# Performance work log

Hardware: AMD Instinct MI355X
Metric: run time of the kernel (lower is better)

Reference implementation:

```python
import jax, jax.numpy as jnp
import numpy as np

B = 16          # frames in batch
N = 16384       # atoms (num_nodes)
R = 1024        # residues (segments)
D = 320         # input_dim
BINS = 32       # adaptive-pool feature bins (output_size_per_segment[1])
H = 512         # mlp_hidden_dim
COND = 3        # conditioner dim (X_ref)
EPS = 1e-5


def setup_inputs() -> dict:
    key = jax.random.key(0)
    ks = jax.random.split(key, 8)
    x = jax.random.normal(ks[0], (B * N, D), dtype=jnp.float32)
    cond = jax.random.normal(ks[1], (N, COND), dtype=jnp.float32)
    # sorted residue ids -> contiguous variable-size segments, like real residues
    seg_ids = jnp.sort(jax.random.randint(ks[2], (N,), 0, R, dtype=jnp.int32))
    W1 = jax.random.normal(ks[3], (BINS + COND, H), dtype=jnp.float32) * 0.05
    b1 = jnp.zeros((H,), jnp.float32)
    gamma = jnp.ones((H,), jnp.float32)
    beta = jnp.zeros((H,), jnp.float32)
    bn_mean = jnp.zeros((H,), jnp.float32)
    bn_var = jnp.ones((H,), jnp.float32)
    W2 = jax.random.normal(ks[4], (H, 3), dtype=jnp.float32) * 0.05
    b2 = jnp.zeros((3,), jnp.float32)
    return {"x": x, "cond": cond, "seg_ids": seg_ids, "W1": W1, "b1": b1,
            "gamma": gamma, "beta": beta, "bn_mean": bn_mean, "bn_var": bn_var,
            "W2": W2, "b2": b2}


def reference(x, cond, seg_ids, W1, b1, gamma, beta, bn_mean, bn_var, W2, b2):
    # x: [B*N, D] atom embeddings
    x3 = x.reshape(B, N, D)
    # --- per-residue AdaptiveAvgPool2d((1, BINS)) as a fused segment mean ---
    # output height 1 == mean over all atoms of the residue
    counts = jax.ops.segment_sum(jnp.ones((N,), x.dtype), seg_ids, num_segments=R)
    sums = jax.vmap(lambda xb: jax.ops.segment_sum(xb, seg_ids, num_segments=R))(x3)  # [B,R,D]
    seg_mean = sums / jnp.maximum(counts, 1.0)[None, :, None]
    # adaptive width D -> BINS (D divisible by BINS => exact chunk means)
    pooled = seg_mean.reshape(B, R, BINS, D // BINS).mean(-1)  # [B,R,BINS]
    # --- broadcast residue feature back to atoms, concat conditioner ---
    per_atom = pooled[:, seg_ids, :]                           # [B,N,BINS]
    cond_b = jnp.broadcast_to(cond[None], (B, N, COND))
    feat = jnp.concatenate([per_atom, cond_b], axis=-1).reshape(B * N, BINS + COND)
    # --- decoder MLP: Linear -> ReLU -> BatchNorm1d(eval) -> Linear ---
    h = jnp.maximum(feat @ W1 + b1, 0.0)
    h = (h - bn_mean) * jax.lax.rsqrt(bn_var + EPS) * gamma + beta
    out = h @ W2 + b2                                          # [B*N, 3]
    return out
```

## Files before the change

### kernel.cpp

```cpp
#include <hip/hip_runtime.h>
#include <math.h>

#define B_ 16
#define N_ 16384
#define R_ 1024
#define D_ 320
#define BINS_ 32
#define H_ 512
#define EPS_ 1e-5f
#define AP 516
#define EP 260

__global__ __launch_bounds__(256) void k_prep(const int* __restrict__ seg,
                      const float* __restrict__ gamma, const float* __restrict__ beta,
                      const float* __restrict__ mean, const float* __restrict__ var,
                      const float* __restrict__ W2, const float* __restrict__ b2,
                      int* __restrict__ off, float* __restrict__ W2f,
                      float* __restrict__ bias3, float* __restrict__ pooled){
  __shared__ float red[3 * 256];
  int blk = blockIdx.x, tid = threadIdx.x;
  if (blk < 5){
    int g = blk * 256 + tid;
    if (g <= R_){
      int lo = 0, hi = N_;
      while (lo < hi){ int mid = (lo + hi) >> 1; if (seg[mid] < g) lo = mid + 1; else hi = mid; }
      off[g] = lo;
    }
  } else if (blk == 5){
    float p0 = 0.f, p1 = 0.f, p2 = 0.f;
    for (int h = tid; h < H_; h += 256){
      float c = gamma[h] / sqrtf(var[h] + EPS_);
      float d = beta[h] - mean[h] * c;
      float w0 = W2[h * 3 + 0], w1 = W2[h * 3 + 1], w2 = W2[h * 3 + 2];
      W2f[h * 3 + 0] = c * w0; W2f[h * 3 + 1] = c * w1; W2f[h * 3 + 2] = c * w2;
      p0 += d * w0; p1 += d * w1; p2 += d * w2;
    }
    red[tid] = p0; red[256 + tid] = p1; red[512 + tid] = p2;
    __syncthreads();
    for (int s = 128; s > 0; s >>= 1){
      if (tid < s){
        red[tid] += red[tid + s];
        red[256 + tid] += red[256 + tid + s];
        red[512 + tid] += red[512 + tid + s];
      }
      __syncthreads();
    }
    if (tid < 3) bias3[tid] = b2[tid] + red[tid * 256];
  } else {
    float4 z = {0.f, 0.f, 0.f, 0.f};
    float4* p4 = (float4*)pooled;
    const int total4 = B_ * R_ * BINS_ / 4;
    for (int i = (blk - 6) * 256 + tid; i < total4; i += 32 * 256) p4[i] = z;
  }
}

__global__ __launch_bounds__(256) void k_pool(const float* __restrict__ x,
                                              const int* __restrict__ seg,
                                              float* __restrict__ pooled){
  __shared__ __align__(16) float red[4 * 320];
  int tid = threadIdx.x;
  int wid = tid >> 6, lane = tid & 63;
  int c = blockIdx.x * 4 + wid;
  int b = blockIdx.y;
  int base = c * 64;
  int my_seg = seg[base + lane];
  int prev = __shfl_up(my_seg, 1);
  bool bnd = (lane == 0) || (my_seg != prev);
  unsigned long long mask = __ballot(bnd);
  const float* xp = x + ((size_t)b * N_ + base) * D_ + lane;
  float* wred = &red[wid * 320];
  while (mask){
    int i = __builtin_ctzll(mask);
    mask &= mask - 1;
    int e = mask ? __builtin_ctzll(mask) : 64;
    int sg = __shfl(my_seg, i);
    float a0 = 0.f, a1 = 0.f, a2 = 0.f, a3 = 0.f, a4 = 0.f;
    const float* rp = xp + (size_t)i * D_;
    for (int r = i; r < e; r++, rp += D_){
      a0 += rp[0]; a1 += rp[64]; a2 += rp[128]; a3 += rp[192]; a4 += rp[256];
    }
    wred[lane] = a0; wred[64 + lane] = a1; wred[128 + lane] = a2;
    wred[192 + lane] = a3; wred[256 + lane] = a4;
    if (lane < 32){
      float s = 0.f;
      #pragma unroll
      for (int j = 0; j < 10; j++) s += wred[lane * 10 + j];
      atomicAdd(&pooled[((size_t)b * R_ + sg) * BINS_ + lane], s);
    }
  }
}

__global__ __launch_bounds__(256) void k_main(const float* __restrict__ pooled, const float* __restrict__ cond,
                      const float* __restrict__ W1, const float* __restrict__ b1,
                      const int* __restrict__ off, const float* __restrict__ W2f,
                      const float* __restrict__ bias3, float* __restrict__ out){
  __shared__ __align__(16) float P[B_ * BINS_];
  __shared__ __align__(16) float A[B_ * AP];
  __shared__ __align__(16) float E[16 * EP];
  __shared__ float condT[16 * 3];
  int tid = threadIdx.x;
  int r = blockIdx.x;
  int s = off[r];
  int cnt = off[r + 1] - s;
  if (cnt == 0) return;

  float sc = 1.0f / (float)(cnt * 10);
  for (int i = tid; i < B_ * BINS_; i += 256)
    P[i] = pooled[(size_t)((i >> 5) * R_ + r) * BINS_ + (i & 31)] * sc;
  __syncthreads();

  for (int h = tid; h < H_; h += 256){
    float bb = b1[h];
    float acc[B_];
    #pragma unroll
    for (int b = 0; b < B_; b++) acc[b] = bb;
    #pragma unroll
    for (int k = 0; k < BINS_; k++){
      float w = W1[k * H_ + h];
      #pragma unroll
      for (int b = 0; b < B_; b++) acc[b] += P[b * BINS_ + k] * w;
    }
    #pragma unroll
    for (int b = 0; b < B_; b++) A[b * AP + h] = acc[b];
  }

  int a = tid >> 4, b = tid & 15;
  for (int t0 = 0; t0 < cnt; t0 += 16){
    int na = min(16, cnt - t0);
    __syncthreads();
    if (tid < 48){
      int aa = tid / 3, cc = tid % 3;
      condT[tid] = (aa < na) ? cond[(size_t)(s + t0 + aa) * 3 + cc] : 0.f;
    }
    __syncthreads();
    float o0 = 0.f, o1 = 0.f, o2 = 0.f;
    int ae = a < na ? a : 0;
    for (int hc = 0; hc < 2; hc++){
      int h = (hc << 8) + tid;
      float w0 = W1[32 * H_ + h], w1 = W1[33 * H_ + h], w2 = W1[34 * H_ + h];
      for (int aa = 0; aa < na; aa++)
        E[aa * EP + tid] = condT[aa * 3] * w0 + condT[aa * 3 + 1] * w1 + condT[aa * 3 + 2] * w2;
      __syncthreads();
      const float* Ap = &A[b * AP + (hc << 8)];
      const float* Ep = &E[ae * EP];
      const float* Wp = &W2f[(hc << 8) * 3];
      #pragma unroll 4
      for (int hp = 0; hp < 256; hp += 4){
        float4 av = *(const float4*)(Ap + hp);
        float4 ev = *(const float4*)(Ep + hp);
        const float* w = Wp + hp * 3;
        float z;
        z = av.x + ev.x; z = fmaxf(z, 0.f); o0 = fmaf(z, w[0], o0); o1 = fmaf(z, w[1], o1); o2 = fmaf(z, w[2], o2);
        z = av.y + ev.y; z = fmaxf(z, 0.f); o0 = fmaf(z, w[3], o0); o1 = fmaf(z, w[4], o1); o2 = fmaf(z, w[5], o2);
        z = av.z + ev.z; z = fmaxf(z, 0.f); o0 = fmaf(z, w[6], o0); o1 = fmaf(z, w[7], o1); o2 = fmaf(z, w[8], o2);
        z = av.w + ev.w; z = fmaxf(z, 0.f); o0 = fmaf(z, w[9], o0); o1 = fmaf(z, w[10], o1); o2 = fmaf(z, w[11], o2);
      }
      __syncthreads();
    }
    if (a < na){
      size_t oi = ((size_t)b * N_ + (size_t)(s + t0 + a)) * 3;
      out[oi + 0] = o0 + bias3[0];
      out[oi + 1] = o1 + bias3[1];
      out[oi + 2] = o2 + bias3[2];
    }
  }
}

extern "C" void kernel_launch(void* const* d_in, const int* in_sizes, int n_in,
                              void* d_out, int out_size, void* d_ws, size_t ws_size,
                              hipStream_t stream) {
  const float* x      = (const float*)d_in[0];
  const float* cond   = (const float*)d_in[1];
  const int*   seg    = (const int*)  d_in[2];
  const float* W1     = (const float*)d_in[3];
  const float* b1     = (const float*)d_in[4];
  const float* gamma  = (const float*)d_in[5];
  const float* beta   = (const float*)d_in[6];
  const float* bnmean = (const float*)d_in[7];
  const float* bnvar  = (const float*)d_in[8];
  const float* W2     = (const float*)d_in[9];
  const float* b2     = (const float*)d_in[10];
  float* out = (float*)d_out;

  char* ws = (char*)d_ws;
  int*   seg_off = (int*)ws;
  float* W2f     = (float*)(ws + 8192);
  float* bias3   = (float*)(ws + 14592);
  float* pooled  = (float*)(ws + 16384);

  k_prep<<<dim3(38), dim3(256), 0, stream>>>(seg, gamma, beta, bnmean, bnvar, W2, b2,
                                             seg_off, W2f, bias3, pooled);
  k_pool<<<dim3(N_ / 64 / 4, B_), dim3(256), 0, stream>>>(x, seg, pooled);
  k_main<<<dim3(R_), dim3(256), 0, stream>>>(pooled, cond, W1, b1, seg_off, W2f, bias3, out);
}
```

Measured before the change: 634.8 us.

## Split residue feature GEMM into tiled kernel and vectorize pooling loads

The per-residue pooled-features times W1 product moves out of k_main into a new register-tiled GEMM kernel (k_feat). It writes a [R*B, H] activation buffer to workspace, and k_main then loads that buffer into shared memory. Separately, k_pool switches to float4 loads for the first 256 columns of each row. The aim is better FMA reuse in the small GEMM and wider memory transactions in the bandwidth-bound pooling pass, at the cost of an extra launch and an extra global round trip of about 32 MB.

```diff
diff --git a/kernel.cpp b/kernel.cpp
--- a/kernel.cpp
+++ b/kernel.cpp
@@ -67,20 +67,24 @@
   int prev = __shfl_up(my_seg, 1);
   bool bnd = (lane == 0) || (my_seg != prev);
   unsigned long long mask = __ballot(bnd);
-  const float* xp = x + ((size_t)b * N_ + base) * D_ + lane;
+  const float* xp = x + ((size_t)b * N_ + base) * D_;
   float* wred = &red[wid * 320];
   while (mask){
     int i = __builtin_ctzll(mask);
     mask &= mask - 1;
     int e = mask ? __builtin_ctzll(mask) : 64;
     int sg = __shfl(my_seg, i);
-    float a0 = 0.f, a1 = 0.f, a2 = 0.f, a3 = 0.f, a4 = 0.f;
-    const float* rp = xp + (size_t)i * D_;
-    for (int r = i; r < e; r++, rp += D_){
-      a0 += rp[0]; a1 += rp[64]; a2 += rp[128]; a3 += rp[192]; a4 += rp[256];
-    }
-    wred[lane] = a0; wred[64 + lane] = a1; wred[128 + lane] = a2;
-    wred[192 + lane] = a3; wred[256 + lane] = a4;
+    float4 a0 = {0.f, 0.f, 0.f, 0.f};
+    float a4 = 0.f;
+    const float* rp  = xp + (size_t)i * D_ + 4 * lane;
+    const float* rp1 = xp + (size_t)i * D_ + 256 + lane;
+    for (int r = i; r < e; r++, rp += D_, rp1 += D_){
+      float4 v = *(const float4*)rp;
+      a0.x += v.x; a0.y += v.y; a0.z += v.z; a0.w += v.w;
+      a4 += *rp1;
+    }
+    *(float4*)&wred[4 * lane] = a0;
+    wred[256 + lane] = a4;
     if (lane < 32){
       float s = 0.f;
       #pragma unroll
@@ -90,11 +94,61 @@
   }
 }
 
-__global__ __launch_bounds__(256) void k_main(const float* __restrict__ pooled, const float* __restrict__ cond,
+__global__ __launch_bounds__(256) void k_feat(const float* __restrict__ pooled,
                       const float* __restrict__ W1, const float* __restrict__ b1,
+                      const int* __restrict__ off, float* __restrict__ Ag){
+  __shared__ float Pt[64][33];
+  __shared__ __align__(16) float Wt[32][64];
+  int tid = threadIdx.x;
+  int c0 = blockIdx.x * 64;
+  int m0 = blockIdx.y * 64;
+  for (int i = tid; i < 64 * 32; i += 256){
+    int row = i >> 5, k = i & 31;
+    int m = m0 + row;
+    int r = m >> 4, b = m & 15;
+    int cnt = off[r + 1] - off[r];
+    float sc = 1.0f / (10.0f * (float)(cnt > 0 ? cnt : 1));
+    Pt[row][k] = pooled[(size_t)(b * R_ + r) * BINS_ + k] * sc;
+  }
+  for (int i = tid; i < 32 * 64; i += 256){
+    int k = i >> 6, cc = i & 63;
+    Wt[k][cc] = W1[k * H_ + c0 + cc];
+  }
+  __syncthreads();
+  int ty = tid >> 4, tx = tid & 15;
+  float acc[4][4];
+  #pragma unroll
+  for (int i = 0; i < 4; i++)
+    #pragma unroll
+    for (int j = 0; j < 4; j++) acc[i][j] = 0.f;
+  #pragma unroll
+  for (int k = 0; k < 32; k++){
+    float4 wv = *(const float4*)&Wt[k][tx * 4];
+    float p0 = Pt[ty * 4 + 0][k];
+    float p1 = Pt[ty * 4 + 1][k];
+    float p2 = Pt[ty * 4 + 2][k];
+    float p3 = Pt[ty * 4 + 3][k];
+    acc[0][0] = fmaf(p0, wv.x, acc[0][0]); acc[0][1] = fmaf(p0, wv.y, acc[0][1]);
+    acc[0][2] = fmaf(p0, wv.z, acc[0][2]); acc[0][3] = fmaf(p0, wv.w, acc[0][3]);
+    acc[1][0] = fmaf(p1, wv.x, acc[1][0]); acc[1][1] = fmaf(p1, wv.y, acc[1][1]);
+    acc[1][2] = fmaf(p1, wv.z, acc[1][2]); acc[1][3] = fmaf(p1, wv.w, acc[1][3]);
+    acc[2][0] = fmaf(p2, wv.x, acc[2][0]); acc[2][1] = fmaf(p2, wv.y, acc[2][1]);
+    acc[2][2] = fmaf(p2, wv.z, acc[2][2]); acc[2][3] = fmaf(p2, wv.w, acc[2][3]);
+    acc[3][0] = fmaf(p3, wv.x, acc[3][0]); acc[3][1] = fmaf(p3, wv.y, acc[3][1]);
+    acc[3][2] = fmaf(p3, wv.z, acc[3][2]); acc[3][3] = fmaf(p3, wv.w, acc[3][3]);
+  }
+  float4 bv = *(const float4*)&b1[c0 + tx * 4];
+  #pragma unroll
+  for (int i = 0; i < 4; i++){
+    float4 o = {acc[i][0] + bv.x, acc[i][1] + bv.y, acc[i][2] + bv.z, acc[i][3] + bv.w};
+    *(float4*)&Ag[(size_t)(m0 + ty * 4 + i) * H_ + c0 + tx * 4] = o;
+  }
+}
+
+__global__ __launch_bounds__(256) void k_main(const float* __restrict__ Ag, const float* __restrict__ cond,
+                      const float* __restrict__ W1,
                       const int* __restrict__ off, const float* __restrict__ W2f,
                       const float* __restrict__ bias3, float* __restrict__ out){
-  __shared__ __align__(16) float P[B_ * BINS_];
   __shared__ __align__(16) float A[B_ * AP];
   __shared__ __align__(16) float E[16 * EP];
   __shared__ float condT[16 * 3];
@@ -104,24 +158,10 @@
   int cnt = off[r + 1] - s;
   if (cnt == 0) return;
 
-  float sc = 1.0f / (float)(cnt * 10);
-  for (int i = tid; i < B_ * BINS_; i += 256)
-    P[i] = pooled[(size_t)((i >> 5) * R_ + r) * BINS_ + (i & 31)] * sc;
-  __syncthreads();
-
-  for (int h = tid; h < H_; h += 256){
-    float bb = b1[h];
-    float acc[B_];
-    #pragma unroll
-    for (int b = 0; b < B_; b++) acc[b] = bb;
-    #pragma unroll
-    for (int k = 0; k < BINS_; k++){
-      float w = W1[k * H_ + h];
-      #pragma unroll
-      for (int b = 0; b < B_; b++) acc[b] += P[b * BINS_ + k] * w;
-    }
-    #pragma unroll
-    for (int b = 0; b < B_; b++) A[b * AP + h] = acc[b];
+  const float4* Ag4 = (const float4*)(Ag + (size_t)r * (B_ * H_));
+  for (int i = tid; i < B_ * H_ / 4; i += 256){
+    int b = i >> 7, h4 = i & 127;
+    *(float4*)&A[b * AP + h4 * 4] = Ag4[i];
   }
 
   int a = tid >> 4, b = tid & 15;
@@ -187,9 +227,11 @@
   float* W2f     = (float*)(ws + 8192);
   float* bias3   = (float*)(ws + 14592);
   float* pooled  = (float*)(ws + 16384);
+  float* Ag      = (float*)(ws + (4u << 20));
 
   k_prep<<<dim3(38), dim3(256), 0, stream>>>(seg, gamma, beta, bnmean, bnvar, W2, b2,
                                              seg_off, W2f, bias3, pooled);
   k_pool<<<dim3(N_ / 64 / 4, B_), dim3(256), 0, stream>>>(x, seg, pooled);
-  k_main<<<dim3(R_), dim3(256), 0, stream>>>(pooled, cond, W1, b1, seg_off, W2f, bias3, out);
-}
+  k_feat<<<dim3(8, 256), dim3(256), 0, stream>>>(pooled, W1, b1, seg_off, Ag);
+  k_main<<<dim3(R_), dim3(256), 0, stream>>>(Ag, cond, W1, seg_off, W2f, bias3, out);
+}
```

Result: faster. 561.6 us (-11.5%).
